# Kernel tuning notes

Measured on AMD Instinct MI355X. Metric: run time of the kernel, lower is better.

The kernel has to match this reference:

```python
import jax, jax.numpy as jnp
import numpy as np

N_NODES = 100000


def gcn_conv(x, W, b, src, dst, n_nodes):
    """PyG-style GCNConv: add self-loops, symmetric D^-1/2 (A+I) D^-1/2 normalization,
    linear transform, scatter-add aggregation, bias."""
    h = x @ W  # [N, out]
    # add self-loops
    loop = jnp.arange(n_nodes, dtype=src.dtype)
    src_all = jnp.concatenate([src, loop])
    dst_all = jnp.concatenate([dst, loop])
    # degree (of A + I) counted at destination nodes
    deg = jax.ops.segment_sum(jnp.ones_like(dst_all, dtype=h.dtype), dst_all,
                              num_segments=n_nodes)
    dinv = jnp.where(deg > 0, jax.lax.rsqrt(deg), 0.0)  # [N]
    w = dinv[src_all] * dinv[dst_all]                   # per-edge norm
    msg = h[src_all] * w[:, None]                       # gather + scale
    out = jax.ops.segment_sum(msg, dst_all, num_segments=n_nodes)
    return out + b


def setup_inputs() -> dict:
    key = jax.random.key(0)
    k1, k2, k3, k4 = jax.random.split(key, 4)
    n, e = N_NODES, 1600000
    d_in, d_hid, d_out = 128, 128, 64
    x = jax.random.normal(k1, (n, d_in), dtype=jnp.float32)
    edge_index = jax.random.randint(k2, (2, e), 0, n, dtype=jnp.int64)
    W1 = jax.random.normal(k3, (d_in, d_hid), dtype=jnp.float32) / np.sqrt(d_in)
    b1 = jnp.zeros((d_hid,), dtype=jnp.float32)
    W2 = jax.random.normal(k4, (d_hid, d_out), dtype=jnp.float32) / np.sqrt(d_hid)
    b2 = jnp.zeros((d_out,), dtype=jnp.float32)
    return {"x": x, "edge_index": edge_index, "W1": W1, "b1": b1, "W2": W2, "b2": b2}


def reference(x, edge_index, W1, b1, W2, b2):
    src, dst = edge_index[0], edge_index[1]
    h = jax.nn.relu(gcn_conv(x, W1, b1, src, dst, N_NODES))
    return gcn_conv(h, W2, b2, src, dst, N_NODES)
```

## Files before the change

kernel.cpp:

```cpp
#include <hip/hip_runtime.h>
#include <hip/hip_fp16.h>


typedef _Float16 half8 __attribute__((ext_vector_type(8)));
typedef float f32x4 __attribute__((ext_vector_type(4)));

constexpr int BK_SHIFT = 7;
constexpr int BK_NODES = 1 << BK_SHIFT;
constexpr int NB_MAX   = 1024;
constexpr int SLAB     = 2560;
constexpr int P1_EPT   = 32;
constexpr int P1_EDGES = 256 * P1_EPT;

__global__ __launch_bounds__(256) void k_p1(const int* __restrict__ src,
                                            const int* __restrict__ dst, int E,
                                            int NB, int* __restrict__ bfill,
                                            unsigned* __restrict__ slab) {
  __shared__ unsigned stage[P1_EDGES];
  __shared__ unsigned short bidp[P1_EDGES];
  __shared__ int hist[NB_MAX];
  __shared__ int lbase[NB_MAX];
  __shared__ int goff[NB_MAX];
  __shared__ int part[256];

  const int t = threadIdx.x;
  const long base = (long)blockIdx.x * P1_EDGES;
  const int nval = (int)(((long)E - base < (long)P1_EDGES) ? (E - base) : P1_EDGES);

  for (int i = t; i < NB; i += 256) hist[i] = 0;
  __syncthreads();

  int eb[P1_EPT];
  unsigned ev[P1_EPT];
#pragma unroll
  for (int i = 0; i < P1_EPT; ++i) {
    long e = base + t + i * 256;
    int b = -1;
    unsigned v = 0;
    if (e < E) {
      int d = dst[e];
      int s = src[e];
      b = d >> BK_SHIFT;
      v = ((unsigned)(d & (BK_NODES - 1)) << 17) | (unsigned)s;
      atomicAdd(&hist[b], 1);
    }
    eb[i] = b;
    ev[i] = v;
  }
  __syncthreads();

  int lc[4];
  int lsum = 0;
#pragma unroll
  for (int j = 0; j < 4; ++j) {
    int b = t * 4 + j;
    lc[j] = (b < NB) ? hist[b] : 0;
    lsum += lc[j];
  }
  part[t] = lsum;
  __syncthreads();
  for (int o = 1; o < 256; o <<= 1) {
    int a = (t >= o) ? part[t - o] : 0;
    __syncthreads();
    part[t] += a;
    __syncthreads();
  }
  int run = part[t] - lsum;
#pragma unroll
  for (int j = 0; j < 4; ++j) {
    int b = t * 4 + j;
    if (b < NB) lbase[b] = run;
    run += lc[j];
  }
  __syncthreads();

  for (int b = t; b < NB; b += 256) {
    int len = hist[b];
    int g = len ? atomicAdd(&bfill[b], len) : 0;
    goff[b] = b * SLAB + g - lbase[b];
  }
  __syncthreads();

#pragma unroll
  for (int i = 0; i < P1_EPT; ++i) {
    if (eb[i] >= 0) {
      int p = atomicAdd(&lbase[eb[i]], 1);
      stage[p] = ev[i];
      bidp[p] = (unsigned short)eb[i];
    }
  }
  __syncthreads();

  for (int p = t; p < nval; p += 256) {
    int b = bidp[p];
    slab[goff[b] + p] = stage[p];
  }
}

__global__ __launch_bounds__(1024) void k_bscan(const int* __restrict__ bfill, int NB,
                                                int* __restrict__ bbase) {
  __shared__ int sm[1024];
  const int t = threadIdx.x;
  int v = (t < NB) ? bfill[t] : 0;
  sm[t] = v;
  __syncthreads();
  for (int o = 1; o < 1024; o <<= 1) {
    int a = (t >= o) ? sm[t - o] : 0;
    __syncthreads();
    sm[t] += a;
    __syncthreads();
  }
  if (t < NB) bbase[t] = sm[t] - v;
}

__global__ __launch_bounds__(256) void k_p2(const unsigned* __restrict__ slab,
                                            const int* __restrict__ bfill,
                                            const int* __restrict__ bbase, int N,
                                            int* __restrict__ deg,
                                            int* __restrict__ row_ptr,
                                            float* __restrict__ dinv,
                                            int* __restrict__ ssrc) {
  __shared__ int hist[BK_NODES];
  __shared__ int lb[BK_NODES];
  const int b = blockIdx.x;
  const int t = threadIdx.x;
  const int len = bfill[b];
  const int gbase = bbase[b];
  const unsigned* seg = slab + (size_t)b * SLAB;

  if (t < BK_NODES) hist[t] = 0;
  __syncthreads();
  for (int i = t; i < len; i += 256) atomicAdd(&hist[seg[i] >> 17], 1);
  __syncthreads();

  if (t < BK_NODES) lb[t] = hist[t];
  __syncthreads();
  for (int o = 1; o < BK_NODES; o <<= 1) {
    int a = 0;
    if (t < BK_NODES && t >= o) a = lb[t - o];
    __syncthreads();
    if (t < BK_NODES) lb[t] += a;
    __syncthreads();
  }

  int n = b * BK_NODES + t;
  if (t < BK_NODES && n < N) {
    int d = hist[t];
    deg[n] = d;
    row_ptr[n] = gbase + lb[t] - d;
    dinv[n] = rsqrtf((float)(d + 1));
  }
  __syncthreads();
  if (t < BK_NODES) lb[t] -= hist[t];
  __syncthreads();

  for (int i = t; i < len; i += 256) {
    unsigned v = seg[i];
    int l = v >> 17;
    int p = atomicAdd(&lb[l], 1);
    ssrc[gbase + p] = (int)(v & 0x1FFFF);
  }
}

__global__ __launch_bounds__(256) void k_prep(const float* __restrict__ W1,
                                              const float* __restrict__ W2,
                                              __half* __restrict__ Wt1,
                                              __half* __restrict__ Wt2) {
  int i = blockIdx.x * blockDim.x + threadIdx.x;
  if (i < 16384) {
    int k = i >> 7, n = i & 127;
    Wt1[n * 128 + k] = __float2half(W1[i]);
  } else if (i < 24576) {
    int j = i - 16384;
    int k = j >> 6, n = j & 63;
    Wt2[n * 128 + k] = __float2half(W2[j]);
  }
}

template <int NC>
__global__ __launch_bounds__(256) void k_gemm(const float* __restrict__ X,
                                              const __half* __restrict__ Wt,
                                              const float* __restrict__ dinv,
                                              __half* __restrict__ H, int N) {
  constexpr int K = 128;
  constexpr int BM = 64;
  constexpr int LDK = K + 8;
  constexpr int NT = NC / 16;
  __shared__ _Float16 xs[BM * LDK];
  __shared__ _Float16 wl[NC * LDK];

  const int t = threadIdx.x;
  const int r0 = blockIdx.x * BM;

  for (int i = t; i < BM * (K / 4); i += 256) {
    int row = i >> 5, kg = i & 31;
    float4 v = make_float4(0.f, 0.f, 0.f, 0.f);
    if (r0 + row < N)
      v = *reinterpret_cast<const float4*>(X + (size_t)(r0 + row) * K + 4 * kg);
    union { _Float16 h[4]; unsigned long long u; } pk;
    pk.h[0] = (_Float16)v.x; pk.h[1] = (_Float16)v.y;
    pk.h[2] = (_Float16)v.z; pk.h[3] = (_Float16)v.w;
    *reinterpret_cast<unsigned long long*>(&xs[row * LDK + 4 * kg]) = pk.u;
  }
  for (int i = t; i < NC * (K / 8); i += 256) {
    int n = i >> 4, kc = i & 15;
    float4 raw = *reinterpret_cast<const float4*>(Wt + (size_t)n * K + 8 * kc);
    *reinterpret_cast<float4*>(&wl[n * LDK + 8 * kc]) = raw;
  }
  __syncthreads();

  const int w = t >> 6;
  const int lane = t & 63;
  const int lm = lane & 15;
  const int lg = lane >> 4;

  half8 a[4];
#pragma unroll
  for (int kt = 0; kt < 4; ++kt)
    a[kt] = *reinterpret_cast<const half8*>(&xs[(w * 16 + lm) * LDK + kt * 32 + lg * 8]);

  f32x4 acc[NT];
#pragma unroll
  for (int nt = 0; nt < NT; ++nt) acc[nt] = (f32x4){0.f, 0.f, 0.f, 0.f};

#pragma unroll
  for (int nt = 0; nt < NT; ++nt) {
#pragma unroll
    for (int kt = 0; kt < 4; ++kt) {
      half8 b = *reinterpret_cast<const half8*>(
          &wl[(nt * 16 + lm) * LDK + kt * 32 + lg * 8]);
      acc[nt] = __builtin_amdgcn_mfma_f32_16x16x32_f16(a[kt], b, acc[nt], 0, 0, 0);
    }
  }

  float dv[4];
#pragma unroll
  for (int r = 0; r < 4; ++r) {
    int row = r0 + w * 16 + lg * 4 + r;
    dv[r] = (row < N) ? dinv[row] : 0.f;
  }
#pragma unroll
  for (int nt = 0; nt < NT; ++nt) {
#pragma unroll
    for (int r = 0; r < 4; ++r) {
      int row = r0 + w * 16 + lg * 4 + r;
      if (row < N)
        H[(size_t)row * NC + nt * 16 + lm] = __float2half(acc[nt][r] * dv[r]);
    }
  }
}

template <bool RELU>
__global__ __launch_bounds__(256) void k_agg128(const __half* __restrict__ H,
                                                const int* __restrict__ row_ptr,
                                                const int* __restrict__ deg,
                                                const int* __restrict__ ssrc,
                                                const float* __restrict__ dinv,
                                                const float* __restrict__ bias,
                                                float* __restrict__ out, int N) {
  const int wave = threadIdx.x >> 6;
  const int lane = threadIdx.x & 63;
  const int n = blockIdx.x * 4 + wave;
  if (n >= N) return;

  const int eh = lane >> 4;
  const int cl = lane & 15;
  const int e0 = row_ptr[n];
  const int e1 = e0 + deg[n];
  const float dv = dinv[n];

  float acc[8] = {0.f, 0.f, 0.f, 0.f, 0.f, 0.f, 0.f, 0.f};
  auto gat = [&](int s) {
    float4 raw = *reinterpret_cast<const float4*>(H + (size_t)s * 128 + 8 * cl);
    const __half2* hp = reinterpret_cast<const __half2*>(&raw);
#pragma unroll
    for (int j = 0; j < 4; ++j) {
      float2 f = __half22float2(hp[j]);
      acc[2 * j] += f.x;
      acc[2 * j + 1] += f.y;
    }
  };
  if (eh == 0) gat(n);
  int e = e0;
  for (; e + 8 <= e1; e += 8) {
    int sA = ssrc[e + eh];
    int sB = ssrc[e + 4 + eh];
    gat(sA);
    gat(sB);
  }
  if (e + 4 <= e1) { gat(ssrc[e + eh]); e += 4; }
  if (e + eh < e1) gat(ssrc[e + eh]);

#pragma unroll
  for (int j = 0; j < 8; ++j) {
    acc[j] += __shfl_xor(acc[j], 16);
    acc[j] += __shfl_xor(acc[j], 32);
  }
  if (eh == 0) {
    float4 b0 = *reinterpret_cast<const float4*>(bias + 8 * cl);
    float4 b1 = *reinterpret_cast<const float4*>(bias + 8 * cl + 4);
    float4 o0 = make_float4(acc[0] * dv + b0.x, acc[1] * dv + b0.y,
                            acc[2] * dv + b0.z, acc[3] * dv + b0.w);
    float4 o1 = make_float4(acc[4] * dv + b1.x, acc[5] * dv + b1.y,
                            acc[6] * dv + b1.z, acc[7] * dv + b1.w);
    if (RELU) {
      o0.x = fmaxf(o0.x, 0.f); o0.y = fmaxf(o0.y, 0.f);
      o0.z = fmaxf(o0.z, 0.f); o0.w = fmaxf(o0.w, 0.f);
      o1.x = fmaxf(o1.x, 0.f); o1.y = fmaxf(o1.y, 0.f);
      o1.z = fmaxf(o1.z, 0.f); o1.w = fmaxf(o1.w, 0.f);
    }
    *reinterpret_cast<float4*>(out + (size_t)n * 128 + 8 * cl) = o0;
    *reinterpret_cast<float4*>(out + (size_t)n * 128 + 8 * cl + 4) = o1;
  }
}

__global__ __launch_bounds__(256) void k_agg64(const __half* __restrict__ H,
                                               const int* __restrict__ row_ptr,
                                               const int* __restrict__ deg,
                                               const int* __restrict__ ssrc,
                                               const float* __restrict__ dinv,
                                               const float* __restrict__ bias,
                                               float* __restrict__ out, int N) {
  const int wave = threadIdx.x >> 6;
  const int lane = threadIdx.x & 63;
  const int n = blockIdx.x * 4 + wave;
  if (n >= N) return;

  const int eh = lane >> 3;
  const int cl = lane & 7;
  const int e0 = row_ptr[n];
  const int e1 = e0 + deg[n];
  const float dv = dinv[n];

  float acc[8] = {0.f, 0.f, 0.f, 0.f, 0.f, 0.f, 0.f, 0.f};
  auto gat = [&](int s) {
    float4 raw = *reinterpret_cast<const float4*>(H + (size_t)s * 64 + 8 * cl);
    const __half2* hp = reinterpret_cast<const __half2*>(&raw);
#pragma unroll
    for (int j = 0; j < 4; ++j) {
      float2 f = __half22float2(hp[j]);
      acc[2 * j] += f.x;
      acc[2 * j + 1] += f.y;
    }
  };
  if (eh == 0) gat(n);
  int e = e0;
  for (; e + 16 <= e1; e += 16) {
    int sA = ssrc[e + eh];
    int sB = ssrc[e + 8 + eh];
    gat(sA);
    gat(sB);
  }
  if (e + 8 <= e1) { gat(ssrc[e + eh]); e += 8; }
  if (e + eh < e1) gat(ssrc[e + eh]);

#pragma unroll
  for (int j = 0; j < 8; ++j) {
    acc[j] += __shfl_xor(acc[j], 8);
    acc[j] += __shfl_xor(acc[j], 16);
    acc[j] += __shfl_xor(acc[j], 32);
  }
  if (eh == 0) {
    float4 b0 = *reinterpret_cast<const float4*>(bias + 8 * cl);
    float4 b1 = *reinterpret_cast<const float4*>(bias + 8 * cl + 4);
    float4 o0 = make_float4(acc[0] * dv + b0.x, acc[1] * dv + b0.y,
                            acc[2] * dv + b0.z, acc[3] * dv + b0.w);
    float4 o1 = make_float4(acc[4] * dv + b1.x, acc[5] * dv + b1.y,
                            acc[6] * dv + b1.z, acc[7] * dv + b1.w);
    *reinterpret_cast<float4*>(out + (size_t)n * 64 + 8 * cl) = o0;
    *reinterpret_cast<float4*>(out + (size_t)n * 64 + 8 * cl + 4) = o1;
  }
}

extern "C" void kernel_launch(void* const* d_in, const int* in_sizes, int n_in,
                              void* d_out, int out_size, void* d_ws, size_t ws_size,
                              hipStream_t stream) {
  const float* x = (const float*)d_in[0];
  const int* ei = (const int*)d_in[1];
  const float* W1 = (const float*)d_in[2];
  const float* b1 = (const float*)d_in[3];
  const float* W2 = (const float*)d_in[4];
  const float* b2 = (const float*)d_in[5];

  const int K = 128;
  const int N = in_sizes[0] / K;
  const int E = in_sizes[1] / 2;
  const int NB = (N + BK_NODES - 1) >> BK_SHIFT;
  if (NB > NB_MAX) return;

  const int* src = ei;
  const int* dst = ei + E;

  size_t off = 0;
  auto carve = [&](size_t bytes) {
    size_t o = off;
    off += (bytes + 255) & ~(size_t)255;
    return o;
  };
  char* ws = (char*)d_ws;
  int*      deg     = (int*)(ws + carve((size_t)N * 4));
  int*      row_ptr = (int*)(ws + carve((size_t)N * 4));
  float*    dinv    = (float*)(ws + carve((size_t)N * 4));
  int*      bfill   = (int*)(ws + carve((size_t)NB * 4));
  int*      bbase   = (int*)(ws + carve((size_t)NB * 4));
  __half*   wt1     = (__half*)(ws + carve(16384 * 2));
  __half*   wt2     = (__half*)(ws + carve(8192 * 2));
  unsigned* slab    = (unsigned*)(ws + carve((size_t)NB * SLAB * 4));
  int*      ssrc    = (int*)(ws + carve((size_t)E * 4));
  __half*   h1      = (__half*)(ws + carve((size_t)N * K * 2));
  float*    out1    = (float*)(ws + carve((size_t)N * K * 4));
  if (off > ws_size) return;

  __half* h2 = h1;
  float* out2 = (float*)d_out;

  hipMemsetAsync(bfill, 0, (size_t)NB * 4, stream);
  k_prep<<<96, 256, 0, stream>>>(W1, W2, wt1, wt2);
  const int nwg1 = (E + P1_EDGES - 1) / P1_EDGES;
  k_p1<<<nwg1, 256, 0, stream>>>(src, dst, E, NB, bfill, slab);
  k_bscan<<<1, 1024, 0, stream>>>(bfill, NB, bbase);
  k_p2<<<NB, 256, 0, stream>>>(slab, bfill, bbase, N, deg, row_ptr, dinv, ssrc);

  k_gemm<128><<<(N + 63) / 64, 256, 0, stream>>>(x, wt1, dinv, h1, N);
  k_agg128<true><<<(N + 3) / 4, 256, 0, stream>>>(h1, row_ptr, deg, ssrc, dinv,
                                                  b1, out1, N);
  k_gemm<64><<<(N + 63) / 64, 256, 0, stream>>>(out1, wt2, dinv, h2, N);
  k_agg64<<<(N + 3) / 4, 256, 0, stream>>>(h2, row_ptr, deg, ssrc, dinv,
                                           b2, out2, N);
  (void)n_in; (void)out_size;
}
```

Baseline: 207.6 us.

## Slice GEMM output into 16-column feature slabs and aggregate each slice separately

The GEMM now writes H as column slices of 16 halves per node (slice-major), so each slice is a compact N×32-byte array. A new aggregation kernel runs one grid portion per slice, with 16 edges handled in parallel by 4-lane groups and each wave covering 8 nodes. The aim is a per-slice gather working set small enough to stay in L2/MALL, which should raise the cache hit rate on random neighbour gathers. In exchange, the edge list and row pointers are re-read once per slice, and each gather is only 8 bytes, which may lower memory efficiency.

Result: slower. 491.2 us (+136.6%).

```diff
diff --git a/kernel.cpp b/kernel.cpp
--- a/kernel.cpp
+++ b/kernel.cpp
@@ -181,7 +181,7 @@
 __global__ __launch_bounds__(256) void k_gemm(const float* __restrict__ X,
                                               const __half* __restrict__ Wt,
                                               const float* __restrict__ dinv,
-                                              __half* __restrict__ H, int N) {
+                                              __half* __restrict__ Hs, int N) {
   constexpr int K = 128;
   constexpr int BM = 64;
   constexpr int LDK = K + 8;
@@ -245,130 +245,77 @@
     for (int r = 0; r < 4; ++r) {
       int row = r0 + w * 16 + lg * 4 + r;
       if (row < N)
-        H[(size_t)row * NC + nt * 16 + lm] = __float2half(acc[nt][r] * dv[r]);
-    }
-  }
-}
-
-template <bool RELU>
-__global__ __launch_bounds__(256) void k_agg128(const __half* __restrict__ H,
-                                                const int* __restrict__ row_ptr,
-                                                const int* __restrict__ deg,
-                                                const int* __restrict__ ssrc,
-                                                const float* __restrict__ dinv,
-                                                const float* __restrict__ bias,
-                                                float* __restrict__ out, int N) {
+        Hs[(size_t)nt * N * 16 + (size_t)row * 16 + lm] =
+            __float2half(acc[nt][r] * dv[r]);
+    }
+  }
+}
+
+template <int C, int NSL, bool RELU>
+__global__ __launch_bounds__(256) void k_aggs(const __half* __restrict__ Hs,
+                                              const int* __restrict__ rp,
+                                              const int* __restrict__ dg,
+                                              const int* __restrict__ ssrc,
+                                              const float* __restrict__ dinv,
+                                              const float* __restrict__ bias,
+                                              float* __restrict__ out, int N) {
+  constexpr int LOG = (NSL == 8) ? 3 : 2;
+  constexpr int NPW = 8;
   const int wave = threadIdx.x >> 6;
   const int lane = threadIdx.x & 63;
-  const int n = blockIdx.x * 4 + wave;
-  if (n >= N) return;
-
-  const int eh = lane >> 4;
-  const int cl = lane & 15;
-  const int e0 = row_ptr[n];
-  const int e1 = e0 + deg[n];
-  const float dv = dinv[n];
-
-  float acc[8] = {0.f, 0.f, 0.f, 0.f, 0.f, 0.f, 0.f, 0.f};
-  auto gat = [&](int s) {
-    float4 raw = *reinterpret_cast<const float4*>(H + (size_t)s * 128 + 8 * cl);
-    const __half2* hp = reinterpret_cast<const __half2*>(&raw);
+  const int slice = blockIdx.x & (NSL - 1);
+  const int g = blockIdx.x >> LOG;
+  const int eh = lane >> 2;
+  const int cl = lane & 3;
+  const __half* slabp = Hs + (size_t)slice * N * 16;
+  const float4 bv = *reinterpret_cast<const float4*>(bias + slice * 16 + 4 * cl);
+
+  const int n0 = (g * 4 + wave) * NPW;
+  for (int ni = 0; ni < NPW; ++ni) {
+    const int n = n0 + ni;
+    if (n >= N) return;
+    const int e0 = rp[n];
+    const int e1 = e0 + dg[n];
+
+    float acc[4] = {0.f, 0.f, 0.f, 0.f};
+    auto gat = [&](int s) {
+      uint2 raw = *reinterpret_cast<const uint2*>(slabp + (size_t)s * 16 + cl * 4);
+      float2 fa = __half22float2(*reinterpret_cast<__half2*>(&raw.x));
+      float2 fb = __half22float2(*reinterpret_cast<__half2*>(&raw.y));
+      acc[0] += fa.x; acc[1] += fa.y; acc[2] += fb.x; acc[3] += fb.y;
+    };
+    if (eh == 0) gat(n);
+    int e = e0;
+    for (; e + 16 <= e1; e += 16) {
+      int s = __builtin_nontemporal_load(ssrc + e + eh);
+      gat(s);
+    }
+    if (e + eh < e1) {
+      int s = __builtin_nontemporal_load(ssrc + e + eh);
+      gat(s);
+    }
+
 #pragma unroll
     for (int j = 0; j < 4; ++j) {
-      float2 f = __half22float2(hp[j]);
-      acc[2 * j] += f.x;
-      acc[2 * j + 1] += f.y;
-    }
-  };
-  if (eh == 0) gat(n);
-  int e = e0;
-  for (; e + 8 <= e1; e += 8) {
-    int sA = ssrc[e + eh];
-    int sB = ssrc[e + 4 + eh];
-    gat(sA);
-    gat(sB);
-  }
-  if (e + 4 <= e1) { gat(ssrc[e + eh]); e += 4; }
-  if (e + eh < e1) gat(ssrc[e + eh]);
-
-#pragma unroll
-  for (int j = 0; j < 8; ++j) {
-    acc[j] += __shfl_xor(acc[j], 16);
-    acc[j] += __shfl_xor(acc[j], 32);
-  }
-  if (eh == 0) {
-    float4 b0 = *reinterpret_cast<const float4*>(bias + 8 * cl);
-    float4 b1 = *reinterpret_cast<const float4*>(bias + 8 * cl + 4);
-    float4 o0 = make_float4(acc[0] * dv + b0.x, acc[1] * dv + b0.y,
-                            acc[2] * dv + b0.z, acc[3] * dv + b0.w);
-    float4 o1 = make_float4(acc[4] * dv + b1.x, acc[5] * dv + b1.y,
-                            acc[6] * dv + b1.z, acc[7] * dv + b1.w);
-    if (RELU) {
-      o0.x = fmaxf(o0.x, 0.f); o0.y = fmaxf(o0.y, 0.f);
-      o0.z = fmaxf(o0.z, 0.f); o0.w = fmaxf(o0.w, 0.f);
-      o1.x = fmaxf(o1.x, 0.f); o1.y = fmaxf(o1.y, 0.f);
-      o1.z = fmaxf(o1.z, 0.f); o1.w = fmaxf(o1.w, 0.f);
-    }
-    *reinterpret_cast<float4*>(out + (size_t)n * 128 + 8 * cl) = o0;
-    *reinterpret_cast<float4*>(out + (size_t)n * 128 + 8 * cl + 4) = o1;
-  }
-}
-
-__global__ __launch_bounds__(256) void k_agg64(const __half* __restrict__ H,
-                                               const int* __restrict__ row_ptr,
-                                               const int* __restrict__ deg,
-                                               const int* __restrict__ ssrc,
-                                               const float* __restrict__ dinv,
-                                               const float* __restrict__ bias,
-                                               float* __restrict__ out, int N) {
-  const int wave = threadIdx.x >> 6;
-  const int lane = threadIdx.x & 63;
-  const int n = blockIdx.x * 4 + wave;
-  if (n >= N) return;
-
-  const int eh = lane >> 3;
-  const int cl = lane & 7;
-  const int e0 = row_ptr[n];
-  const int e1 = e0 + deg[n];
-  const float dv = dinv[n];
-
-  float acc[8] = {0.f, 0.f, 0.f, 0.f, 0.f, 0.f, 0.f, 0.f};
-  auto gat = [&](int s) {
-    float4 raw = *reinterpret_cast<const float4*>(H + (size_t)s * 64 + 8 * cl);
-    const __half2* hp = reinterpret_cast<const __half2*>(&raw);
-#pragma unroll
-    for (int j = 0; j < 4; ++j) {
-      float2 f = __half22float2(hp[j]);
-      acc[2 * j] += f.x;
-      acc[2 * j + 1] += f.y;
-    }
-  };
-  if (eh == 0) gat(n);
-  int e = e0;
-  for (; e + 16 <= e1; e += 16) {
-    int sA = ssrc[e + eh];
-    int sB = ssrc[e + 8 + eh];
-    gat(sA);
-    gat(sB);
-  }
-  if (e + 8 <= e1) { gat(ssrc[e + eh]); e += 8; }
-  if (e + eh < e1) gat(ssrc[e + eh]);
-
-#pragma unroll
-  for (int j = 0; j < 8; ++j) {
-    acc[j] += __shfl_xor(acc[j], 8);
-    acc[j] += __shfl_xor(acc[j], 16);
-    acc[j] += __shfl_xor(acc[j], 32);
-  }
-  if (eh == 0) {
-    float4 b0 = *reinterpret_cast<const float4*>(bias + 8 * cl);
-    float4 b1 = *reinterpret_cast<const float4*>(bias + 8 * cl + 4);
-    float4 o0 = make_float4(acc[0] * dv + b0.x, acc[1] * dv + b0.y,
-                            acc[2] * dv + b0.z, acc[3] * dv + b0.w);
-    float4 o1 = make_float4(acc[4] * dv + b1.x, acc[5] * dv + b1.y,
-                            acc[6] * dv + b1.z, acc[7] * dv + b1.w);
-    *reinterpret_cast<float4*>(out + (size_t)n * 64 + 8 * cl) = o0;
-    *reinterpret_cast<float4*>(out + (size_t)n * 64 + 8 * cl + 4) = o1;
+      acc[j] += __shfl_xor(acc[j], 4);
+      acc[j] += __shfl_xor(acc[j], 8);
+      acc[j] += __shfl_xor(acc[j], 16);
+      acc[j] += __shfl_xor(acc[j], 32);
+    }
+    if (eh == 0) {
+      const float dv = dinv[n];
+      f32x4 o;
+      o[0] = acc[0] * dv + bv.x;
+      o[1] = acc[1] * dv + bv.y;
+      o[2] = acc[2] * dv + bv.z;
+      o[3] = acc[3] * dv + bv.w;
+      if (RELU) {
+        o[0] = fmaxf(o[0], 0.f); o[1] = fmaxf(o[1], 0.f);
+        o[2] = fmaxf(o[2], 0.f); o[3] = fmaxf(o[3], 0.f);
+      }
+      __builtin_nontemporal_store(
+          o, reinterpret_cast<f32x4*>(out + (size_t)n * C + slice * 16 + cl * 4));
+    }
   }
 }
 
@@ -414,18 +361,19 @@
   __half* h2 = h1;
   float* out2 = (float*)d_out;
 
-  hipMemsetAsync(bfill, 0, (size_t)NB * 4, stream);
+  (void)hipMemsetAsync(bfill, 0, (size_t)NB * 4, stream);
   k_prep<<<96, 256, 0, stream>>>(W1, W2, wt1, wt2);
   const int nwg1 = (E + P1_EDGES - 1) / P1_EDGES;
   k_p1<<<nwg1, 256, 0, stream>>>(src, dst, E, NB, bfill, slab);
   k_bscan<<<1, 1024, 0, stream>>>(bfill, NB, bbase);
   k_p2<<<NB, 256, 0, stream>>>(slab, bfill, bbase, N, deg, row_ptr, dinv, ssrc);
 
+  const int bps = (N + 31) / 32;
   k_gemm<128><<<(N + 63) / 64, 256, 0, stream>>>(x, wt1, dinv, h1, N);
-  k_agg128<true><<<(N + 3) / 4, 256, 0, stream>>>(h1, row_ptr, deg, ssrc, dinv,
-                                                  b1, out1, N);
+  k_aggs<128, 8, true><<<bps * 8, 256, 0, stream>>>(h1, row_ptr, deg, ssrc, dinv,
+                                                    b1, out1, N);
   k_gemm<64><<<(N + 63) / 64, 256, 0, stream>>>(out1, wt2, dinv, h2, N);
-  k_agg64<<<(N + 3) / 4, 256, 0, stream>>>(h2, row_ptr, deg, ssrc, dinv,
-                                           b2, out2, N);
+  k_aggs<64, 4, false><<<bps * 4, 256, 0, stream>>>(h2, row_ptr, deg, ssrc, dinv,
+                                                    b2, out2, N);
   (void)n_in; (void)out_size;
 }
```
